# Kernel tuning notes

Measured on AMD Instinct MI355X. Metric: run time of the kernel, lower is better.

## Reference

```python
import jax, jax.numpy as jnp
import numpy as np

V, E = 50000, 800000
NODE_IN, EDGE_IN, OUT, HEADS = 128, 16, 32, 4
NEG_SLOPE = 0.2  # DGL EdgeGATConv default negative_slope


def setup_inputs() -> dict:
    key = jax.random.key(0)
    ks = jax.random.split(key, 10)
    return {
        "node_feats": jax.random.normal(ks[0], (V, NODE_IN), jnp.float32),
        "edge_feats": jax.random.normal(ks[1], (E, EDGE_IN), jnp.float32),
        "src": jax.random.randint(ks[2], (E,), 0, V),
        "dst": jax.random.randint(ks[3], (E,), 0, V),
        "W_node": jax.random.normal(ks[4], (NODE_IN, HEADS * OUT), jnp.float32) * 0.05,
        "W_edge": jax.random.normal(ks[5], (EDGE_IN, HEADS * OUT), jnp.float32) * 0.05,
        "attn_l": jax.random.normal(ks[6], (HEADS, OUT), jnp.float32) * 0.05,
        "attn_r": jax.random.normal(ks[7], (HEADS, OUT), jnp.float32) * 0.05,
        "attn_e": jax.random.normal(ks[8], (HEADS, OUT), jnp.float32) * 0.05,
        "res_W": jax.random.normal(ks[9], (NODE_IN, HEADS * OUT), jnp.float32) * 0.05,
        "bias": jnp.zeros((HEADS * OUT,), jnp.float32),
    }


def _leaky_relu(x, slope):
    return jnp.where(x >= 0, x, slope * x)


def reference(node_feats, edge_feats, src, dst, W_node, W_edge, attn_l, attn_r, attn_e, res_W, bias):
    V = node_feats.shape[0]
    H, F = attn_l.shape
    # linear projections
    ft = (node_feats @ W_node).reshape(V, H, F)    # [V,H,F]
    fe = (edge_feats @ W_edge).reshape(-1, H, F)   # [E,H,F]
    # per-head attention logits
    el = jnp.einsum('vhf,hf->vh', ft, attn_l)      # [V,H]
    er = jnp.einsum('vhf,hf->vh', ft, attn_r)      # [V,H]
    ee = jnp.einsum('ehf,hf->eh', fe, attn_e)      # [E,H]
    e = _leaky_relu(el[src] + er[dst] + ee, NEG_SLOPE)  # [E,H]
    # edge softmax over incoming edges of each destination node (stable)
    emax = jax.ops.segment_max(e, dst, num_segments=V)  # [V,H]
    ex = jnp.exp(e - emax[dst])
    esum = jax.ops.segment_sum(ex, dst, num_segments=V)  # [V,H]
    a = ex / esum[dst]                                   # [E,H]
    # weighted message passing: u_mul_e(ft, a) then sum to dst
    msg = ft[src] * a[:, :, None]                        # [E,H,F]
    rst = jax.ops.segment_sum(msg, dst, num_segments=V)  # [V,H,F]
    # residual connection + bias (EdgeGATConv residual=True, bias=True)
    rst = rst + (node_feats @ res_W).reshape(V, H, F)
    rst = rst + bias.reshape(1, H, F)
    # agg_mode='flatten': concat heads
    return rst.reshape(V, H * F)
```

## Files before the change

### kernel.cpp

```cpp
#include <hip/hip_runtime.h>
#include <hip/hip_fp16.h>
#include <cstdint>

#define V_N 50000
#define E_N 800000
#define NODE_IN 128
#define EDGE_IN 16
#define HF 128
#define NEG_SLOPE 0.2f
#define NBUCKET 196
#define NPART 784
#define CAP 8192
#define NODE_BLKS 1563
#define PREP_BLKS 64

#define OFF_FT    0
#define OFF_EL    3200000
#define OFF_ER    3400000
#define OFF_ROW   3600000
#define OFF_H     3650260
#define OFF_BSUM  3803924
#define OFF_WATT  3804180
#define OFF_BFRAG 3804244
#define OFF_RECB  3820628
#define OFF_REC   10243156

typedef short bf16x8 __attribute__((ext_vector_type(8)));
typedef float f32x4 __attribute__((ext_vector_type(4)));

__device__ __forceinline__ unsigned short f2bf(float f) {
    unsigned u = __float_as_uint(f);
    u += 0x7fffu + ((u >> 16) & 1u);
    return (unsigned short)(u >> 16);
}
__device__ __forceinline__ unsigned pk2(float lo, float hi) {
    return (unsigned)f2bf(lo) | ((unsigned)f2bf(hi) << 16);
}
__device__ __forceinline__ float bflo(unsigned w) { return __uint_as_float(w << 16); }
__device__ __forceinline__ float bfhi(unsigned w) { return __uint_as_float(w & 0xffff0000u); }

typedef __fp16 fp16x2 __attribute__((ext_vector_type(2)));
__device__ __forceinline__ unsigned pkh2(float a, float b) {
    fp16x2 h = __builtin_amdgcn_cvt_pkrtz(a, b);
    return __builtin_bit_cast(unsigned, h);
}
__device__ __forceinline__ __half2 u2h(unsigned u) {
    return __builtin_bit_cast(__half2, u);
}
__device__ __forceinline__ unsigned h2u(__half2 h) {
    return __builtin_bit_cast(unsigned, h);
}

__global__ __launch_bounds__(256) void k_prephist(
    const float* __restrict__ We, const float* __restrict__ attn_e,
    const float* __restrict__ Wn, const float* __restrict__ Wr,
    const int* __restrict__ dst,
    float* __restrict__ watt, unsigned* __restrict__ bfrag,
    int* __restrict__ H)
{
    const int t = threadIdx.x;
    if (blockIdx.x >= PREP_BLKS) {
        int hb = blockIdx.x - PREP_BLKS;
        __shared__ int h[NBUCKET];
        for (int i = t; i < NBUCKET; i += 256) h[i] = 0;
        __syncthreads();
        #pragma unroll
        for (int c = 0; c < 4; c++) {
            int e = hb * 1024 + c * 256 + t;
            if (e < E_N) atomicAdd(&h[dst[e] >> 8], 1);
        }
        __syncthreads();
        for (int i = t; i < NBUCKET; i += 256) H[i * NPART + hb] = h[i];
        return;
    }
    int g = blockIdx.x * 256 + t;
    if (blockIdx.x == 0 && t < 64) {
        int k = t >> 2, hh = t & 3;
        float s = 0.f;
        #pragma unroll
        for (int f = 0; f < 32; f++)
            s += We[k * HF + hh * 32 + f] * attn_e[hh * 32 + f];
        watt[k * 4 + hh] = s;
    }
    {
        int c    = g >> 8;
        int lane = (g >> 2) & 63;
        int jp   = g & 3;
        int nt = c >> 2, ks = c & 3;
        int col = nt * 16 + (lane & 15);
        int k   = ks * 32 + (lane >> 4) * 8 + jp * 2;
        const float* W = (col < 128) ? Wn : Wr;
        int cc = col & 127;
        float x0 = W[(size_t)k * 128 + cc];
        float x1 = W[(size_t)(k + 1) * 128 + cc];
        bfrag[g] = pk2(x0, x1);
    }
}

__global__ __launch_bounds__(256) void k_nodescan(
    const float* __restrict__ nf, const unsigned* __restrict__ bfragw,
    const float* __restrict__ attn_l, const float* __restrict__ attn_r,
    const float* __restrict__ bias,
    unsigned* __restrict__ ftw, float* __restrict__ el,
    float* __restrict__ er, float* __restrict__ out,
    int* __restrict__ H, int* __restrict__ binsum)
{
    __shared__ __align__(16) float sSf[32 * 140];
    unsigned short* sA = (unsigned short*)sSf;

    if (blockIdx.x < NBUCKET) {
        int* shi = (int*)sSf;
        const int bin = blockIdx.x;
        const int t = threadIdx.x;
        const int base = bin * NPART;
        int4 v = {0, 0, 0, 0};
        if (t < NPART / 4) v = *(const int4*)&H[base + t * 4];
        int ls = v.x + v.y + v.z + v.w;
        shi[t] = ls;
        __syncthreads();
        #pragma unroll
        for (int off = 1; off < 256; off <<= 1) {
            int u = (t >= off) ? shi[t - off] : 0;
            __syncthreads();
            shi[t] += u;
            __syncthreads();
        }
        int exc = shi[t] - ls;
        if (t < NPART / 4) {
            int c0 = bin * CAP + exc;
            int4 o;
            o.x = c0;
            o.y = c0 + v.x;
            o.z = c0 + v.x + v.y;
            o.w = c0 + v.x + v.y + v.z;
            *(int4*)&H[base + t * 4] = o;
        }
        if (t == 255) binsum[bin] = shi[255];
        return;
    }

    const int t = threadIdx.x;
    const int lane = t & 63;
    const int w = t >> 6;
    const int nb = (blockIdx.x - NBUCKET) * 32;
    const int n15 = lane & 15;
    const int q = lane >> 4;
    const unsigned short* bfrag = (const unsigned short*)bfragw;

    #pragma unroll
    for (int i = 0; i < 4; i++) {
        int f = t + i * 256;
        int node = f >> 5;
        int kc = (f & 31) * 4;
        float4 v = {0.f, 0.f, 0.f, 0.f};
        if (nb + node < V_N)
            v = *(const float4*)(nf + (size_t)(nb + node) * NODE_IN + kc);
        uint2 u2 = make_uint2(pk2(v.x, v.y), pk2(v.z, v.w));
        *(uint2*)&sA[node * 136 + kc] = u2;
    }
    __syncthreads();

    f32x4 acc[2][4];
    #pragma unroll
    for (int m = 0; m < 2; m++)
        #pragma unroll
        for (int tt = 0; tt < 4; tt++) acc[m][tt] = (f32x4){0.f, 0.f, 0.f, 0.f};

    #pragma unroll
    for (int ks = 0; ks < 4; ks++) {
        bf16x8 a0 = *(const bf16x8*)&sA[n15 * 136 + ks * 32 + q * 8];
        bf16x8 a1 = *(const bf16x8*)&sA[(16 + n15) * 136 + ks * 32 + q * 8];
        #pragma unroll
        for (int tt = 0; tt < 4; tt++) {
            int nt = (tt < 2) ? (2 * w + tt) : (8 + 2 * w + (tt - 2));
            bf16x8 b = *(const bf16x8*)(bfrag + ((size_t)(nt * 4 + ks) * 64 + lane) * 8);
            acc[0][tt] = __builtin_amdgcn_mfma_f32_16x16x32_bf16(a0, b, acc[0][tt], 0, 0, 0);
            acc[1][tt] = __builtin_amdgcn_mfma_f32_16x16x32_bf16(a1, b, acc[1][tt], 0, 0, 0);
        }
    }

    {
        float al0 = attn_l[w * 32 + n15];
        float al1 = attn_l[w * 32 + 16 + n15];
        float ar0 = attn_r[w * 32 + n15];
        float ar1 = attn_r[w * 32 + 16 + n15];
        #pragma unroll
        for (int m = 0; m < 2; m++) {
            #pragma unroll
            for (int r = 0; r < 4; r++) {
                float fa = acc[m][0][r], fb = acc[m][1][r];
                float elp = fa * al0 + fb * al1;
                float erp = fa * ar0 + fb * ar1;
                elp += __shfl_xor(elp, 1); erp += __shfl_xor(erp, 1);
                elp += __shfl_xor(elp, 2); erp += __shfl_xor(erp, 2);
                elp += __shfl_xor(elp, 4); erp += __shfl_xor(erp, 4);
                elp += __shfl_xor(elp, 8); erp += __shfl_xor(erp, 8);
                int node = nb + m * 16 + q * 4 + r;
                if (n15 == 0 && node < V_N) {
                    el[node * 4 + w] = elp;
                    er[node * 4 + w] = erp;
                }
            }
        }
    }
    #pragma unroll
    for (int m = 0; m < 2; m++)
        #pragma unroll
        for (int r = 0; r < 4; r++) {
            int node = nb + m * 16 + q * 4 + r;
            if (node < V_N)
                ftw[(size_t)node * 64 + w * 16 + n15] =
                    pkh2(acc[m][0][r], acc[m][1][r]);
        }
    __syncthreads();

    #pragma unroll
    for (int m = 0; m < 2; m++)
        #pragma unroll
        for (int tt = 2; tt < 4; tt++)
            #pragma unroll
            for (int r = 0; r < 4; r++)
                sSf[(m * 16 + q * 4 + r) * 140 + w * 32 + (tt - 2) * 16 + n15] =
                    acc[m][tt][r];
    __syncthreads();
    #pragma unroll
    for (int i = 0; i < 4; i++) {
        int u = t + i * 256;
        int node = u >> 5, c4 = (u & 31) * 4;
        if (nb + node < V_N) {
            float4 v = *(float4*)&sSf[node * 140 + c4];
            float4 b4 = *(const float4*)(bias + c4);
            v.x += b4.x; v.y += b4.y; v.z += b4.z; v.w += b4.w;
            *(float4*)(out + (size_t)(nb + node) * HF + c4) = v;
        }
    }
}

__global__ __launch_bounds__(256) void k_bin(
    const float* __restrict__ ef, const int* __restrict__ src,
    const int* __restrict__ dst, const float* __restrict__ watt,
    const float* __restrict__ el, const int* __restrict__ H,
    uint4* __restrict__ recb)
{
    __shared__ float sw[64];
    __shared__ __align__(16) float see[256][4];
    __shared__ int boff[NBUCKET];
    const int t = threadIdx.x;
    const int b = blockIdx.x;
    if (t < 64) sw[t] = watt[t];
    for (int i = t; i < NBUCKET; i += 256) boff[i] = H[i * NPART + b];
    __syncthreads();
    const int lane = t & 63, w = t >> 6;
    const int k0 = (lane & 3) * 4;

    for (int c = 0; c < 4; c++) {
        const int base = b * 1024 + c * 256;
        #pragma unroll
        for (int r = 0; r < 4; r++) {
            int le = w * 64 + r * 16 + (lane >> 2);
            int ge = base + le;
            float4 v = {0.f, 0.f, 0.f, 0.f};
            if (ge < E_N)
                v = *(const float4*)(ef + (size_t)ge * EDGE_IN + k0);
            float e0 = 0.f, e1 = 0.f, e2 = 0.f, e3 = 0.f;
            float vv[4] = {v.x, v.y, v.z, v.w};
            #pragma unroll
            for (int j = 0; j < 4; j++) {
                int k = k0 + j;
                e0 += vv[j] * sw[k * 4 + 0];
                e1 += vv[j] * sw[k * 4 + 1];
                e2 += vv[j] * sw[k * 4 + 2];
                e3 += vv[j] * sw[k * 4 + 3];
            }
            e0 += __shfl_xor(e0, 1); e1 += __shfl_xor(e1, 1);
            e2 += __shfl_xor(e2, 1); e3 += __shfl_xor(e3, 1);
            e0 += __shfl_xor(e0, 2); e1 += __shfl_xor(e1, 2);
            e2 += __shfl_xor(e2, 2); e3 += __shfl_xor(e3, 2);
            if ((lane & 3) == 0) {
                float4 o = {e0, e1, e2, e3};
                *(float4*)&see[le][0] = o;
            }
        }
        __syncthreads();

        int e = base + t;
        if (e < E_N) {
            int s = src[e], d = dst[e];
            int p = atomicAdd(&boff[d >> 8], 1);
            float4 ee = *(float4*)&see[t][0];
            float4 el4 = *(const float4*)(el + (size_t)s * 4);
            uint4 rr;
            rr.x = (unsigned)s;
            rr.y = pk2(el4.x + ee.x, el4.y + ee.y);
            rr.z = pk2(el4.z + ee.z, el4.w + ee.w);
            rr.w = (unsigned)d;
            recb[p] = rr;
        }
        __syncthreads();
    }
}

__global__ __launch_bounds__(256) void k_group(
    const int* __restrict__ binsum, const uint4* __restrict__ recb,
    uint4* __restrict__ rec, int* __restrict__ rowp)
{
    __shared__ int cnt[256];
    __shared__ int s1[256];
    __shared__ int cur[256];
    const int t = threadIdx.x;
    const int b = blockIdx.x;

    int pre = 0;
    for (int i = t; i < b; i += 256) pre += binsum[i];
    s1[t] = pre;
    __syncthreads();
    #pragma unroll
    for (int off = 128; off > 0; off >>= 1) {
        if (t < off) s1[t] += s1[t + off];
        __syncthreads();
    }
    const int gbase = s1[0];
    const int size = binsum[b];
    const int src0 = b * CAP;
    __syncthreads();

    cnt[t] = 0;
    __syncthreads();
    const int* recw = (const int*)recb;
    for (int i = t; i < size; i += 256)
        atomicAdd(&cnt[recw[4 * (src0 + i) + 3] & 255], 1);
    __syncthreads();
    int v = cnt[t];
    s1[t] = v;
    __syncthreads();
    #pragma unroll
    for (int off = 1; off < 256; off <<= 1) {
        int u = (t >= off) ? s1[t - off] : 0;
        __syncthreads();
        s1[t] += u;
        __syncthreads();
    }
    int exc = s1[t] - v;
    int d = (b << 8) + t;
    if (d < V_N) rowp[d] = gbase + exc;
    if (b == 0 && t == 0) rowp[V_N] = E_N;
    cur[t] = gbase + exc;
    __syncthreads();
    for (int i = t; i < size; i += 256) {
        uint4 r = recb[src0 + i];
        int dl = (int)(r.w & 255u);
        int p = atomicAdd(&cur[dl], 1);
        rec[p] = r;
    }
}

__global__ __launch_bounds__(256) void k_gather(
    const int* __restrict__ row, const uint4* __restrict__ rec,
    const float* __restrict__ er,
    const unsigned* __restrict__ ftw, float* __restrict__ out)
{
    __shared__ unsigned aw[16][16][4];
    const int t = threadIdx.x;
    const int g = t >> 4;
    const int li = t & 15;
    const int head = li >> 2;
    const int lanebase = t & 48;
    const int d = blockIdx.x * 16 + g;
    const int n0 = row[d];
    const int deg = row[d + 1] - n0;
    if (deg == 0) return;

    const float4 er4 = *(const float4*)(er + (size_t)d * 4);
    float4 s4 = {0.f, 0.f, 0.f, 0.f};
    __half2 ha0 = u2h(0u), ha1 = u2h(0u), ha2 = u2h(0u), ha3 = u2h(0u);
    __half2 hb0 = u2h(0u), hb1 = u2h(0u), hb2 = u2h(0u), hb3 = u2h(0u);

    for (int i0 = 0; i0 < deg; i0 += 16) {
        int chunk = min(16, deg - i0);
        int si = 0;
        float4 ex = {0.f, 0.f, 0.f, 0.f};
        if (li < chunk) {
            uint4 r = rec[n0 + i0 + li];
            si = (int)r.x;
            float x0 = bflo(r.y) + er4.x;
            float x1 = bfhi(r.y) + er4.y;
            float x2 = bflo(r.z) + er4.z;
            float x3 = bfhi(r.z) + er4.w;
            x0 = x0 >= 0.f ? x0 : NEG_SLOPE * x0;
            x1 = x1 >= 0.f ? x1 : NEG_SLOPE * x1;
            x2 = x2 >= 0.f ? x2 : NEG_SLOPE * x2;
            x3 = x3 >= 0.f ? x3 : NEG_SLOPE * x3;
            ex.x = __expf(x0); ex.y = __expf(x1);
            ex.z = __expf(x2); ex.w = __expf(x3);
            s4.x += ex.x; s4.y += ex.y; s4.z += ex.z; s4.w += ex.w;
        }
        uint4 ap;
        ap.x = pkh2(ex.x, ex.x); ap.y = pkh2(ex.y, ex.y);
        ap.z = pkh2(ex.z, ex.z); ap.w = pkh2(ex.w, ex.w);
        *(uint4*)&aw[g][li][0] = ap;
        asm volatile("s_waitcnt lgkmcnt(0)" ::: "memory");

        int ce = (chunk + 1) & ~1;
        for (int j = 0; j < ce; j += 2) {
            int s0 = __shfl(si, lanebase + j);
            int s1v = __shfl(si, lanebase + j + 1);
            unsigned a0 = aw[g][j][head];
            unsigned a1 = aw[g][j + 1][head];
            uint4 w0 = *(const uint4*)(ftw + (size_t)s0 * 64 + li * 4);
            uint4 w1 = *(const uint4*)(ftw + (size_t)s1v * 64 + li * 4);
            ha0 = __hfma2(u2h(w0.x), u2h(a0), ha0);
            ha1 = __hfma2(u2h(w0.y), u2h(a0), ha1);
            ha2 = __hfma2(u2h(w0.z), u2h(a0), ha2);
            ha3 = __hfma2(u2h(w0.w), u2h(a0), ha3);
            hb0 = __hfma2(u2h(w1.x), u2h(a1), hb0);
            hb1 = __hfma2(u2h(w1.y), u2h(a1), hb1);
            hb2 = __hfma2(u2h(w1.z), u2h(a1), hb2);
            hb3 = __hfma2(u2h(w1.w), u2h(a1), hb3);
        }
    }
    #pragma unroll
    for (int off = 1; off < 16; off <<= 1) {
        s4.x += __shfl_xor(s4.x, off);
        s4.y += __shfl_xor(s4.y, off);
        s4.z += __shfl_xor(s4.z, off);
        s4.w += __shfl_xor(s4.w, off);
    }
    ha0 = __hadd2(ha0, hb0); ha1 = __hadd2(ha1, hb1);
    ha2 = __hadd2(ha2, hb2); ha3 = __hadd2(ha3, hb3);

    float rsv = 1.f / (head == 0 ? s4.x : head == 1 ? s4.y :
                       head == 2 ? s4.z : s4.w);
    float* op = out + (size_t)d * HF + head * 32 + (li & 3) * 4;
    float4 r0 = *(float4*)op;
    r0.x += __low2float(ha0) * rsv; r0.y += __low2float(ha1) * rsv;
    r0.z += __low2float(ha2) * rsv; r0.w += __low2float(ha3) * rsv;
    *(float4*)op = r0;
    float4 r1 = *(float4*)(op + 16);
    r1.x += __high2float(ha0) * rsv; r1.y += __high2float(ha1) * rsv;
    r1.z += __high2float(ha2) * rsv; r1.w += __high2float(ha3) * rsv;
    *(float4*)(op + 16) = r1;
}

extern "C" void kernel_launch(void* const* d_in, const int* in_sizes, int n_in,
                              void* d_out, int out_size, void* d_ws, size_t ws_size,
                              hipStream_t stream) {
    const float* nf     = (const float*)d_in[0];
    const float* ef     = (const float*)d_in[1];
    const int*   src    = (const int*)d_in[2];
    const int*   dst    = (const int*)d_in[3];
    const float* Wn     = (const float*)d_in[4];
    const float* We     = (const float*)d_in[5];
    const float* attn_l = (const float*)d_in[6];
    const float* attn_r = (const float*)d_in[7];
    const float* attn_e = (const float*)d_in[8];
    const float* Wr     = (const float*)d_in[9];
    const float* bias   = (const float*)d_in[10];
    float* out = (float*)d_out;

    unsigned* wsw  = (unsigned*)d_ws;
    unsigned* ftw  = wsw + OFF_FT;
    float* el      = (float*)(wsw + OFF_EL);
    float* er      = (float*)(wsw + OFF_ER);
    int* rowp      = (int*)(wsw + OFF_ROW);
    int* H         = (int*)(wsw + OFF_H);
    int* binsum    = (int*)(wsw + OFF_BSUM);
    float* watt    = (float*)(wsw + OFF_WATT);
    unsigned* bfrag = wsw + OFF_BFRAG;
    uint4* recb    = (uint4*)(wsw + OFF_RECB);
    uint4* rec     = (uint4*)(wsw + OFF_REC);

    k_prephist<<<PREP_BLKS + NPART, 256, 0, stream>>>(
        We, attn_e, Wn, Wr, dst, watt, bfrag, H);
    k_nodescan<<<NBUCKET + NODE_BLKS, 256, 0, stream>>>(
        nf, bfrag, attn_l, attn_r, bias, ftw, el, er, out, H, binsum);
    k_bin<<<NPART, 256, 0, stream>>>(ef, src, dst, watt, el, H, recb);
    k_group<<<NBUCKET, 256, 0, stream>>>(binsum, recb, rec, rowp);
    k_gather<<<V_N / 16, 256, 0, stream>>>(rowp, rec, er, ftw, out);
}
```

Baseline: 225.0 us.

## Halve edge partition size and transpose histogram layout for binning kernels

```diff
diff --git a/kernel.cpp b/kernel.cpp
--- a/kernel.cpp
+++ b/kernel.cpp
@@ -9,7 +9,8 @@
 #define HF 128
 #define NEG_SLOPE 0.2f
 #define NBUCKET 196
-#define NPART 784
+#define NPART 1563
+#define PSZ 512
 #define CAP 8192
 #define NODE_BLKS 1563
 #define PREP_BLKS 64
@@ -19,11 +20,11 @@
 #define OFF_ER    3400000
 #define OFF_ROW   3600000
 #define OFF_H     3650260
-#define OFF_BSUM  3803924
-#define OFF_WATT  3804180
-#define OFF_BFRAG 3804244
-#define OFF_RECB  3820628
-#define OFF_REC   10243156
+#define OFF_BSUM  3956608
+#define OFF_WATT  3956864
+#define OFF_BFRAG 3956928
+#define OFF_RECB  3973312
+#define OFF_REC   10395840
 
 typedef short bf16x8 __attribute__((ext_vector_type(8)));
 typedef float f32x4 __attribute__((ext_vector_type(4)));
@@ -65,12 +66,12 @@
         for (int i = t; i < NBUCKET; i += 256) h[i] = 0;
         __syncthreads();
         #pragma unroll
-        for (int c = 0; c < 4; c++) {
-            int e = hb * 1024 + c * 256 + t;
+        for (int c = 0; c < 2; c++) {
+            int e = hb * PSZ + c * 256 + t;
             if (e < E_N) atomicAdd(&h[dst[e] >> 8], 1);
         }
         __syncthreads();
-        for (int i = t; i < NBUCKET; i += 256) H[i * NPART + hb] = h[i];
+        for (int i = t; i < NBUCKET; i += 256) H[hb * NBUCKET + i] = h[i];
         return;
     }
     int g = blockIdx.x * 256 + t;
@@ -112,10 +113,14 @@
         int* shi = (int*)sSf;
         const int bin = blockIdx.x;
         const int t = threadIdx.x;
-        const int base = bin * NPART;
-        int4 v = {0, 0, 0, 0};
-        if (t < NPART / 4) v = *(const int4*)&H[base + t * 4];
-        int ls = v.x + v.y + v.z + v.w;
+        int v[8];
+        int ls = 0;
+        #pragma unroll
+        for (int j = 0; j < 8; j++) {
+            int p = t * 8 + j;
+            v[j] = (p < NPART) ? H[p * NBUCKET + bin] : 0;
+            ls += v[j];
+        }
         shi[t] = ls;
         __syncthreads();
         #pragma unroll
@@ -125,15 +130,11 @@
             shi[t] += u;
             __syncthreads();
         }
-        int exc = shi[t] - ls;
-        if (t < NPART / 4) {
-            int c0 = bin * CAP + exc;
-            int4 o;
-            o.x = c0;
-            o.y = c0 + v.x;
-            o.z = c0 + v.x + v.y;
-            o.w = c0 + v.x + v.y + v.z;
-            *(int4*)&H[base + t * 4] = o;
+        int c = bin * CAP + shi[t] - ls;
+        #pragma unroll
+        for (int j = 0; j < 8; j++) {
+            int p = t * 8 + j;
+            if (p < NPART) { H[p * NBUCKET + bin] = c; c += v[j]; }
         }
         if (t == 255) binsum[bin] = shi[255];
         return;
@@ -243,51 +244,52 @@
     uint4* __restrict__ recb)
 {
     __shared__ float sw[64];
-    __shared__ __align__(16) float see[256][4];
+    __shared__ __align__(16) float see[PSZ][4];
     __shared__ int boff[NBUCKET];
     const int t = threadIdx.x;
     const int b = blockIdx.x;
     if (t < 64) sw[t] = watt[t];
-    for (int i = t; i < NBUCKET; i += 256) boff[i] = H[i * NPART + b];
+    if (t < NBUCKET) boff[t] = H[b * NBUCKET + t];
     __syncthreads();
     const int lane = t & 63, w = t >> 6;
     const int k0 = (lane & 3) * 4;
 
-    for (int c = 0; c < 4; c++) {
-        const int base = b * 1024 + c * 256;
-        #pragma unroll
-        for (int r = 0; r < 4; r++) {
-            int le = w * 64 + r * 16 + (lane >> 2);
-            int ge = base + le;
-            float4 v = {0.f, 0.f, 0.f, 0.f};
-            if (ge < E_N)
-                v = *(const float4*)(ef + (size_t)ge * EDGE_IN + k0);
-            float e0 = 0.f, e1 = 0.f, e2 = 0.f, e3 = 0.f;
-            float vv[4] = {v.x, v.y, v.z, v.w};
-            #pragma unroll
-            for (int j = 0; j < 4; j++) {
-                int k = k0 + j;
-                e0 += vv[j] * sw[k * 4 + 0];
-                e1 += vv[j] * sw[k * 4 + 1];
-                e2 += vv[j] * sw[k * 4 + 2];
-                e3 += vv[j] * sw[k * 4 + 3];
-            }
-            e0 += __shfl_xor(e0, 1); e1 += __shfl_xor(e1, 1);
-            e2 += __shfl_xor(e2, 1); e3 += __shfl_xor(e3, 1);
-            e0 += __shfl_xor(e0, 2); e1 += __shfl_xor(e1, 2);
-            e2 += __shfl_xor(e2, 2); e3 += __shfl_xor(e3, 2);
-            if ((lane & 3) == 0) {
-                float4 o = {e0, e1, e2, e3};
-                *(float4*)&see[le][0] = o;
-            }
-        }
-        __syncthreads();
-
-        int e = base + t;
+    #pragma unroll
+    for (int r = 0; r < 8; r++) {
+        int le = w * 128 + r * 16 + (lane >> 2);
+        int ge = b * PSZ + le;
+        float4 v = {0.f, 0.f, 0.f, 0.f};
+        if (ge < E_N)
+            v = *(const float4*)(ef + (size_t)ge * EDGE_IN + k0);
+        float e0 = 0.f, e1 = 0.f, e2 = 0.f, e3 = 0.f;
+        float vv[4] = {v.x, v.y, v.z, v.w};
+        #pragma unroll
+        for (int j = 0; j < 4; j++) {
+            int k = k0 + j;
+            e0 += vv[j] * sw[k * 4 + 0];
+            e1 += vv[j] * sw[k * 4 + 1];
+            e2 += vv[j] * sw[k * 4 + 2];
+            e3 += vv[j] * sw[k * 4 + 3];
+        }
+        e0 += __shfl_xor(e0, 1); e1 += __shfl_xor(e1, 1);
+        e2 += __shfl_xor(e2, 1); e3 += __shfl_xor(e3, 1);
+        e0 += __shfl_xor(e0, 2); e1 += __shfl_xor(e1, 2);
+        e2 += __shfl_xor(e2, 2); e3 += __shfl_xor(e3, 2);
+        if ((lane & 3) == 0) {
+            float4 o = {e0, e1, e2, e3};
+            *(float4*)&see[le][0] = o;
+        }
+    }
+    __syncthreads();
+
+    #pragma unroll
+    for (int c = 0; c < 2; c++) {
+        int le = c * 256 + t;
+        int e = b * PSZ + le;
         if (e < E_N) {
             int s = src[e], d = dst[e];
             int p = atomicAdd(&boff[d >> 8], 1);
-            float4 ee = *(float4*)&see[t][0];
+            float4 ee = *(float4*)&see[le][0];
             float4 el4 = *(const float4*)(el + (size_t)s * 4);
             uint4 rr;
             rr.x = (unsigned)s;
@@ -296,7 +298,6 @@
             rr.w = (unsigned)d;
             recb[p] = rr;
         }
-        __syncthreads();
     }
 }
 
```

Result: faster. 218.4 us (-2.9%).
